# Optimization experiments

Hardware: AMD Instinct MI355X
Metric: run time of the kernel (lower is better)

Reference implementation:

```python
import jax, jax.numpy as jnp
import numpy as np

DEPTH = 3
UNITS = 512
INNER = 32          # inner_dim == F-1
F = INNER + 1
B, N = 128, 100


def setup_inputs() -> dict:
    key = jax.random.key(0)
    k1, k2, k3, k4, k5 = jax.random.split(key, 5)
    x = jax.random.normal(k1, (B, N, N, F), dtype=jnp.float32)
    # W_inner: identity tiled + small uniform noise (init_inner='identity')
    W_inner = (jnp.tile(jnp.eye(INNER, dtype=jnp.float32)[None], (DEPTH + 1, 1, 1))
               + jax.random.uniform(k2, (DEPTH + 1, INNER, INNER), minval=-0.05, maxval=0.05))
    b_inner = jax.random.uniform(k3, (DEPTH + 1, 1, INNER), minval=-0.05, maxval=0.05)
    # W_output: uniform with scale_output=0.01, tiled across depths; b_output zeros
    W_out_single = jax.random.uniform(k4, (INNER, UNITS), minval=-0.01, maxval=0.01)
    W_output = jnp.tile(W_out_single[None], (DEPTH + 1, 1, 1))
    b_output = jnp.zeros((DEPTH + 1, 1, UNITS), dtype=jnp.float32)
    return {"x": x, "W_inner": W_inner, "b_inner": b_inner,
            "W_output": W_output, "b_output": b_output}


def _fp_contribution(attr, W_output, b_output, d):
    # softmax over the units axis, per atom; attr[:, :-1] is [N, INNER]
    return jax.nn.softmax(attr[:, :-1] @ W_output[d] + b_output[d, 0], axis=-1)


def _single(graph0, W_inner, b_inner, W_output, b_output):
    # graph0: [N, N, F]
    attr = jnp.diagonal(graph0, axis1=0, axis2=1).T            # [N, F]
    fp = _fp_contribution(attr, W_output, b_output, 0).sum(axis=0)
    bonds = graph0[:, :, -1]                                    # [N, N]
    boa_T = (bonds + jnp.eye(bonds.shape[0], dtype=graph0.dtype)).T  # bonds_or_atoms transposed: [i,j]=boa[j,i]
    graph = graph0
    for d in range(1, DEPTH + 1):
        pre = graph.sum(axis=1)                                 # [N, F] row-sums of each feature slice
        core = pre[:, :-1] @ W_inner[d] + b_inner[d, 0]         # linear inner activation
        new_attr = jnp.concatenate([core, attr[:, -1:]], axis=1)  # keep bond channel
        # graph[i,j,f] += boa[j,i] * (new_attr - attr)[i,f]  (rank-1 per atom)
        graph = graph + boa_T[:, :, None] * (new_attr - attr)[:, None, :]
        attr = new_attr
        fp = fp + _fp_contribution(attr, W_output, b_output, d).sum(axis=0)
    return fp


def reference(x, W_inner, b_inner, W_output, b_output):
    return jax.vmap(lambda g: _single(g, W_inner, b_inner, W_output, b_output))(x)  # [B, UNITS]
```

## Files before the change

kernel.cpp:

```cpp
#include <hip/hip_runtime.h>

typedef __attribute__((ext_vector_type(4))) float f32x4;
typedef __attribute__((ext_vector_type(8))) short s16x8;

#define NB 128
#define NA 100
#define KF 32
#define NF 33
#define NU 512
#define ND 3

#define SZ_S0    (NB * NA * KF)
#define SZ_BONDS (NB * NA * NA)

__device__ __forceinline__ unsigned short f2bf(float f) {
    unsigned int u = __float_as_uint(f);
    u = (u + 0x7fffu + ((u >> 16) & 1u)) >> 16;
    return (unsigned short)u;
}
__device__ __forceinline__ float bf2f(unsigned short h) {
    return __uint_as_float(((unsigned int)h) << 16);
}

__global__ __launch_bounds__(256) void p1_reduce(const float* __restrict__ x,
    float* __restrict__ S0, float* __restrict__ attrAll, float* __restrict__ bonds)
{
    const int blk = blockIdx.x;
    const int b   = blk / NA;
    const int i   = blk % NA;
    const int t   = threadIdx.x;

    __shared__ float lds[NA * NF];
    __shared__ float red[8][KF];

    const float4* row4 = (const float4*)(x + (size_t)blk * (NA * NF));
    float4* lds4 = (float4*)lds;
    for (int idx = t; idx < (NA * NF) / 4; idx += 256) lds4[idx] = row4[idx];
    __syncthreads();

    const int g = t >> 5;
    const int f = t & 31;
    float p0 = 0.f, p1 = 0.f;
    for (int j = g; j + 8 < NA; j += 16) {
        p0 += lds[j * NF + f];
        p1 += lds[(j + 8) * NF + f];
    }
    if (g < 4) p0 += lds[(96 + g) * NF + f];
    red[g][f] = p0 + p1;
    __syncthreads();

    if (t < KF) {
        float s = 0.f;
#pragma unroll
        for (int gg = 0; gg < 8; ++gg) s += red[gg][t];
        S0[(size_t)blk * KF + t] = s;
    } else if (t >= 64 && t < 64 + KF) {
        attrAll[(size_t)b * (ND + 1) * NA * KF + (size_t)i * KF + (t - 64)] = lds[i * NF + (t - 64)];
    } else if (t >= 128 && t < 128 + NA) {
        const int j = t - 128;
        bonds[(size_t)blk * NA + j] = lds[j * NF + KF];
    }
}

#define NAH 50
#define ELH (NAH * KF)
__global__ __launch_bounds__(256) void p2a_recur(
    const float* __restrict__ S0, const float* __restrict__ bonds,
    const float* __restrict__ W_inner, const float* __restrict__ b_inner,
    float* __restrict__ attrAll)
{
    __shared__ float S[ELH];
    __shared__ float attr[ELH];
    __shared__ float rs[NAH];

    const int blk  = blockIdx.x;
    const int half = blk & 1;
    const int b    = blk >> 1;
    const int t    = threadIdx.x;
    const int f    = t & 31;

    const float4* s4 = (const float4*)(S0 + (size_t)b * NA * KF + half * ELH);
    const float4* a4 = (const float4*)(attrAll + (size_t)b * (ND + 1) * NA * KF + half * ELH);
    for (int idx = t; idx < ELH / 4; idx += 256) {
        ((float4*)S)[idx]    = s4[idx];
        ((float4*)attr)[idx] = a4[idx];
    }
    if (t < NAH) {
        const int i = half * NAH + t;
        const float* bb = bonds + (size_t)b * NA * NA + i;
        float c0=0.f,c1=0.f,c2=0.f,c3=0.f,c4=0.f,c5=0.f,c6=0.f,c7=0.f;
        int j = 0;
        for (; j + 8 <= NA; j += 8) {
            c0 += bb[(j+0)*NA]; c1 += bb[(j+1)*NA];
            c2 += bb[(j+2)*NA]; c3 += bb[(j+3)*NA];
            c4 += bb[(j+4)*NA]; c5 += bb[(j+5)*NA];
            c6 += bb[(j+6)*NA]; c7 += bb[(j+7)*NA];
        }
        for (; j < NA; ++j) c0 += bb[j*NA];
        rs[t] = 1.f + (((c0+c1)+(c2+c3))+((c4+c5)+(c6+c7)));
    }
    __syncthreads();

    float* attrDst = attrAll + (size_t)b * (ND + 1) * NA * KF + half * ELH;

    for (int d = 1; d <= ND; ++d) {
        float Wc[KF];
        const float* Wd = W_inner + d * KF * KF + f;
#pragma unroll
        for (int k = 0; k < KF; ++k) Wc[k] = Wd[k * KF];
        const float bi = b_inner[d * KF + f];

        float core[7];
#pragma unroll
        for (int it = 0; it < 7; ++it) {
            const int idx = t + it * 256;
            if (idx < ELH) {
                const int row = idx >> 5;
                const float4* Sr4 = (const float4*)(S + row * KF);
                float acc = bi;
#pragma unroll
                for (int q = 0; q < 8; ++q) {
                    const float4 sv = Sr4[q];
                    acc += sv.x * Wc[4*q] + sv.y * Wc[4*q+1]
                         + sv.z * Wc[4*q+2] + sv.w * Wc[4*q+3];
                }
                core[it] = acc;
            }
        }
        __syncthreads();
#pragma unroll
        for (int it = 0; it < 7; ++it) {
            const int idx = t + it * 256;
            if (idx < ELH) {
                const int row = idx >> 5;
                const float cc  = core[it];
                const float old = attr[idx];
                attr[idx] = cc;
                S[idx] += rs[row] * (cc - old);
                attrDst[(size_t)d * NA * KF + idx] = cc;
            }
        }
        __syncthreads();
    }
}

__global__ __launch_bounds__(256) void pW_prep(const float* __restrict__ W_output,
    unsigned short* __restrict__ WBh, unsigned short* __restrict__ WBl)
{
    const int i = blockIdx.x * 256 + threadIdx.x;
    const int d = i >> 14, rem = i & 16383, k = rem >> 9, col = rem & 511;
    const float v = W_output[(size_t)d * (KF * NU) + (size_t)k * NU + col];
    const unsigned short hi = f2bf(v);
    const unsigned short lo = f2bf(v - bf2f(hi));
    const int dst = d * 16384 + (col >> 4) * 512 + (k >> 3) * 128 + (col & 15) * 8 + (k & 7);
    WBh[dst] = hi;
    WBl[dst] = lo;
}

__global__ __launch_bounds__(448) void p2b_mfma(
    const float* __restrict__ attrAll,
    const unsigned short* __restrict__ WBh_g, const unsigned short* __restrict__ WBl_g,
    const float* __restrict__ b_output, float* __restrict__ fpPart)
{
    extern __shared__ unsigned char smraw[];
    unsigned short* WBh  = (unsigned short*)smraw;
    unsigned short* WBl  = WBh + 16384;
    unsigned short* aAh  = WBl + 16384;
    unsigned short* aAl  = aAh + 3584;
    float*          biasL= (float*)(aAl + 3584);
    float*          fpw  = (float*)aAh;

    const int blk = blockIdx.x;
    const int b   = blk & (NB - 1);
    const int d   = blk >> 7;
    const int t   = threadIdx.x;
    const int l   = t & 63;
    const int w   = t >> 6;

    for (int i = t; i < 2048; i += 448) ((float4*)WBh)[i] = ((const float4*)WBh_g)[d * 2048 + i];
    for (int i = t; i < 2048; i += 448) ((float4*)WBl)[i] = ((const float4*)WBl_g)[d * 2048 + i];
    for (int i = t; i < NU; i += 448)   biasL[i] = b_output[d * NU + i];

    const float* A = attrAll + ((size_t)b * (ND + 1) + d) * (NA * KF);
    for (int i = t; i < 3584; i += 448) {
        const int gr = i >> 5, k = i & 31;
        const float v = (gr < NA) ? A[gr * KF + k] : 0.f;
        const unsigned short hi = f2bf(v);
        const unsigned short lo = f2bf(v - bf2f(hi));
        const int dst = ((gr >> 4) * 4 + (k >> 3)) * 128 + (gr & 15) * 8 + (k & 7);
        aAh[dst] = hi;
        aAl[dst] = lo;
    }
    __syncthreads();

    const int aoff = (w * 4 + (l >> 4)) * 128 + (l & 15) * 8;
    const s16x8 ah = *(const s16x8*)&aAh[aoff];
    const s16x8 al = *(const s16x8*)&aAl[aoff];
    __syncthreads();

    const int laneoff = (l >> 4) * 128 + (l & 15) * 8;

    float m[4] = {-1e30f, -1e30f, -1e30f, -1e30f};
#pragma unroll 2
    for (int tt = 0; tt < 32; ++tt) {
        const s16x8 bh = *(const s16x8*)&WBh[tt * 512 + laneoff];
        f32x4 c = {0.f, 0.f, 0.f, 0.f};
        c = __builtin_amdgcn_mfma_f32_16x16x32_bf16(ah, bh, c, 0, 0, 0);
        const float bias = biasL[tt * 16 + (l & 15)];
#pragma unroll
        for (int r = 0; r < 4; ++r) m[r] = fmaxf(m[r], c[r] + bias);
    }
#pragma unroll
    for (int off = 1; off <= 8; off <<= 1)
#pragma unroll
        for (int r = 0; r < 4; ++r) m[r] = fmaxf(m[r], __shfl_xor(m[r], off, 64));

    float s[4] = {0.f, 0.f, 0.f, 0.f};
#pragma unroll 2
    for (int tt = 0; tt < 32; ++tt) {
        const s16x8 bh = *(const s16x8*)&WBh[tt * 512 + laneoff];
        const s16x8 bl = *(const s16x8*)&WBl[tt * 512 + laneoff];
        f32x4 c = {0.f, 0.f, 0.f, 0.f};
        c = __builtin_amdgcn_mfma_f32_16x16x32_bf16(ah, bh, c, 0, 0, 0);
        c = __builtin_amdgcn_mfma_f32_16x16x32_bf16(ah, bl, c, 0, 0, 0);
        c = __builtin_amdgcn_mfma_f32_16x16x32_bf16(al, bh, c, 0, 0, 0);
        const float bias = biasL[tt * 16 + (l & 15)];
#pragma unroll
        for (int r = 0; r < 4; ++r) s[r] += __expf(c[r] + bias - m[r]);
    }
#pragma unroll
    for (int off = 1; off <= 8; off <<= 1)
#pragma unroll
        for (int r = 0; r < 4; ++r) s[r] += __shfl_xor(s[r], off, 64);

    float K[4];
#pragma unroll
    for (int r = 0; r < 4; ++r) {
        const int grow = w * 16 + (l >> 4) * 4 + r;
        K[r] = (grow < NA) ? (m[r] + __logf(s[r])) : 1e30f;
    }

#pragma unroll 2
    for (int tt = 0; tt < 32; ++tt) {
        const s16x8 bh = *(const s16x8*)&WBh[tt * 512 + laneoff];
        const s16x8 bl = *(const s16x8*)&WBl[tt * 512 + laneoff];
        f32x4 c = {0.f, 0.f, 0.f, 0.f};
        c = __builtin_amdgcn_mfma_f32_16x16x32_bf16(ah, bh, c, 0, 0, 0);
        c = __builtin_amdgcn_mfma_f32_16x16x32_bf16(ah, bl, c, 0, 0, 0);
        c = __builtin_amdgcn_mfma_f32_16x16x32_bf16(al, bh, c, 0, 0, 0);
        const float bias = biasL[tt * 16 + (l & 15)];
        float f = 0.f;
#pragma unroll
        for (int r = 0; r < 4; ++r) f += __expf(c[r] + bias - K[r]);
        f += __shfl_xor(f, 16, 64);
        f += __shfl_xor(f, 32, 64);
        if (l < 16) fpw[w * NU + tt * 16 + l] = f;
    }
    __syncthreads();

    for (int u = t; u < NU; u += 448) {
        float sacc = 0.f;
#pragma unroll
        for (int ww = 0; ww < 7; ++ww) sacc += fpw[ww * NU + u];
        fpPart[((size_t)d * NB + b) * NU + u] = sacc;
    }
}

__global__ __launch_bounds__(512) void p2c_out(const float* __restrict__ fpPart,
                                               float* __restrict__ out)
{
    const int b = blockIdx.x, t = threadIdx.x;
    float s = 0.f;
#pragma unroll
    for (int d = 0; d <= ND; ++d) s += fpPart[((size_t)d * NB + b) * NU + t];
    out[(size_t)b * NU + t] = s;
}

extern "C" void kernel_launch(void* const* d_in, const int* in_sizes, int n_in,
                              void* d_out, int out_size, void* d_ws, size_t ws_size,
                              hipStream_t stream) {
    (void)in_sizes; (void)n_in; (void)out_size; (void)ws_size;
    const float* x        = (const float*)d_in[0];
    const float* W_inner  = (const float*)d_in[1];
    const float* b_inner  = (const float*)d_in[2];
    const float* W_output = (const float*)d_in[3];
    const float* b_output = (const float*)d_in[4];
    float* out = (float*)d_out;

    float* S0      = (float*)d_ws;
    float* bonds   = S0 + SZ_S0;
    float* attrAll = bonds + SZ_BONDS;
    float* fpPart  = bonds;
    unsigned short* WBh = (unsigned short*)S0;
    unsigned short* WBl = WBh + 65536;

    p1_reduce<<<NB * NA, 256, 0, stream>>>(x, S0, attrAll, bonds);
    p2a_recur<<<NB * 2, 256, 0, stream>>>(S0, bonds, W_inner, b_inner, attrAll);
    pW_prep<<<256, 256, 0, stream>>>(W_output, WBh, WBl);

    const size_t smemB = 81920;
    hipFuncSetAttribute(reinterpret_cast<const void*>(p2b_mfma),
                        hipFuncAttributeMaxDynamicSharedMemorySize, (int)smemB);
    p2b_mfma<<<NB * (ND + 1), 448, smemB, stream>>>(attrAll, WBh, WBl, b_output, fpPart);
    p2c_out<<<NB, 512, 0, stream>>>(fpPart, out);
}
```

Before: 73.34 us.

## Cache softmax exponentials in registers, fuse weight prep into recurrence kernel

The third MFMA pass that recomputed logits and exponentials is gone. Exponentials from the sum pass are now packed as bf16 pairs in registers and later scaled by the reciprocal row sum, which removes a full set of MFMAs and exps per tile. The W_output bf16 split conversion moves into extra blocks of the recurrence kernel, saving one launch; its buffer is relocated to avoid clobbering S0. This adds register pressure (64 packed values, launch bounds of 4 waves) and lowers the precision of the exponentials to bf16.

Result: faster. 69.94 us (-4.6%).

```diff
diff --git a/kernel.cpp b/kernel.cpp
--- a/kernel.cpp
+++ b/kernel.cpp
@@ -20,6 +20,11 @@
 }
 __device__ __forceinline__ float bf2f(unsigned short h) {
     return __uint_as_float(((unsigned int)h) << 16);
+}
+__device__ __forceinline__ unsigned int pack_bf16(float a, float b) {
+    const unsigned int ua = (__float_as_uint(a) + 0x8000u) >> 16;
+    const unsigned int ub = (__float_as_uint(b) + 0x8000u) & 0xffff0000u;
+    return ua | ub;
 }
 
 __global__ __launch_bounds__(256) void p1_reduce(const float* __restrict__ x,
@@ -67,16 +72,34 @@
 __global__ __launch_bounds__(256) void p2a_recur(
     const float* __restrict__ S0, const float* __restrict__ bonds,
     const float* __restrict__ W_inner, const float* __restrict__ b_inner,
-    float* __restrict__ attrAll)
+    float* __restrict__ attrAll,
+    const float* __restrict__ W_output,
+    unsigned short* __restrict__ WBh, unsigned short* __restrict__ WBl)
 {
+    const int blk = blockIdx.x;
+    const int t   = threadIdx.x;
+
+    if (blk >= NB * 2) {
+        const int base = (blk - NB * 2) * 4096;
+        for (int j = t; j < 4096; j += 256) {
+            const int i = base + j;
+            const int d = i >> 14, rem = i & 16383, k = rem >> 9, col = rem & 511;
+            const float v = W_output[(size_t)d * (KF * NU) + (size_t)k * NU + col];
+            const unsigned short hi = f2bf(v);
+            const unsigned short lo = f2bf(v - bf2f(hi));
+            const int dst = d * 16384 + (col >> 4) * 512 + (k >> 3) * 128 + (col & 15) * 8 + (k & 7);
+            WBh[dst] = hi;
+            WBl[dst] = lo;
+        }
+        return;
+    }
+
     __shared__ float S[ELH];
     __shared__ float attr[ELH];
     __shared__ float rs[NAH];
 
-    const int blk  = blockIdx.x;
     const int half = blk & 1;
     const int b    = blk >> 1;
-    const int t    = threadIdx.x;
     const int f    = t & 31;
 
     const float4* s4 = (const float4*)(S0 + (size_t)b * NA * KF + half * ELH);
@@ -144,20 +167,7 @@
     }
 }
 
-__global__ __launch_bounds__(256) void pW_prep(const float* __restrict__ W_output,
-    unsigned short* __restrict__ WBh, unsigned short* __restrict__ WBl)
-{
-    const int i = blockIdx.x * 256 + threadIdx.x;
-    const int d = i >> 14, rem = i & 16383, k = rem >> 9, col = rem & 511;
-    const float v = W_output[(size_t)d * (KF * NU) + (size_t)k * NU + col];
-    const unsigned short hi = f2bf(v);
-    const unsigned short lo = f2bf(v - bf2f(hi));
-    const int dst = d * 16384 + (col >> 4) * 512 + (k >> 3) * 128 + (col & 15) * 8 + (k & 7);
-    WBh[dst] = hi;
-    WBl[dst] = lo;
-}
-
-__global__ __launch_bounds__(448) void p2b_mfma(
+__global__ __launch_bounds__(448, 4) void p2b_mfma(
     const float* __restrict__ attrAll,
     const unsigned short* __restrict__ WBh_g, const unsigned short* __restrict__ WBl_g,
     const float* __restrict__ b_output, float* __restrict__ fpPart)
@@ -215,8 +225,9 @@
 #pragma unroll
         for (int r = 0; r < 4; ++r) m[r] = fmaxf(m[r], __shfl_xor(m[r], off, 64));
 
+    unsigned int eP[64];
     float s[4] = {0.f, 0.f, 0.f, 0.f};
-#pragma unroll 2
+#pragma unroll
     for (int tt = 0; tt < 32; ++tt) {
         const s16x8 bh = *(const s16x8*)&WBh[tt * 512 + laneoff];
         const s16x8 bl = *(const s16x8*)&WBl[tt * 512 + laneoff];
@@ -225,33 +236,34 @@
         c = __builtin_amdgcn_mfma_f32_16x16x32_bf16(ah, bl, c, 0, 0, 0);
         c = __builtin_amdgcn_mfma_f32_16x16x32_bf16(al, bh, c, 0, 0, 0);
         const float bias = biasL[tt * 16 + (l & 15)];
-#pragma unroll
-        for (int r = 0; r < 4; ++r) s[r] += __expf(c[r] + bias - m[r]);
+        const float e0 = __expf(c[0] + bias - m[0]);
+        const float e1 = __expf(c[1] + bias - m[1]);
+        const float e2 = __expf(c[2] + bias - m[2]);
+        const float e3 = __expf(c[3] + bias - m[3]);
+        s[0] += e0; s[1] += e1; s[2] += e2; s[3] += e3;
+        eP[tt * 2]     = pack_bf16(e0, e1);
+        eP[tt * 2 + 1] = pack_bf16(e2, e3);
     }
 #pragma unroll
     for (int off = 1; off <= 8; off <<= 1)
 #pragma unroll
         for (int r = 0; r < 4; ++r) s[r] += __shfl_xor(s[r], off, 64);
 
-    float K[4];
+    float inv[4];
 #pragma unroll
     for (int r = 0; r < 4; ++r) {
         const int grow = w * 16 + (l >> 4) * 4 + r;
-        K[r] = (grow < NA) ? (m[r] + __logf(s[r])) : 1e30f;
-    }
-
-#pragma unroll 2
+        inv[r] = (grow < NA) ? 1.f / s[r] : 0.f;
+    }
+
+#pragma unroll
     for (int tt = 0; tt < 32; ++tt) {
-        const s16x8 bh = *(const s16x8*)&WBh[tt * 512 + laneoff];
-        const s16x8 bl = *(const s16x8*)&WBl[tt * 512 + laneoff];
-        f32x4 c = {0.f, 0.f, 0.f, 0.f};
-        c = __builtin_amdgcn_mfma_f32_16x16x32_bf16(ah, bh, c, 0, 0, 0);
-        c = __builtin_amdgcn_mfma_f32_16x16x32_bf16(ah, bl, c, 0, 0, 0);
-        c = __builtin_amdgcn_mfma_f32_16x16x32_bf16(al, bh, c, 0, 0, 0);
-        const float bias = biasL[tt * 16 + (l & 15)];
-        float f = 0.f;
-#pragma unroll
-        for (int r = 0; r < 4; ++r) f += __expf(c[r] + bias - K[r]);
+        const unsigned int p01 = eP[tt * 2];
+        const unsigned int p23 = eP[tt * 2 + 1];
+        float f = __uint_as_float(p01 << 16)          * inv[0]
+                + __uint_as_float(p01 & 0xffff0000u)  * inv[1]
+                + __uint_as_float(p23 << 16)          * inv[2]
+                + __uint_as_float(p23 & 0xffff0000u)  * inv[3];
         f += __shfl_xor(f, 16, 64);
         f += __shfl_xor(f, 32, 64);
         if (l < 16) fpw[w * NU + tt * 16 + l] = f;
@@ -291,12 +303,12 @@
     float* bonds   = S0 + SZ_S0;
     float* attrAll = bonds + SZ_BONDS;
     float* fpPart  = bonds;
-    unsigned short* WBh = (unsigned short*)S0;
+    unsigned short* WBh = (unsigned short*)(attrAll + (size_t)NB * (ND + 1) * NA * KF);
     unsigned short* WBl = WBh + 65536;
 
     p1_reduce<<<NB * NA, 256, 0, stream>>>(x, S0, attrAll, bonds);
-    p2a_recur<<<NB * 2, 256, 0, stream>>>(S0, bonds, W_inner, b_inner, attrAll);
-    pW_prep<<<256, 256, 0, stream>>>(W_output, WBh, WBl);
+    p2a_recur<<<NB * 2 + 16, 256, 0, stream>>>(S0, bonds, W_inner, b_inner, attrAll,
+                                               W_output, WBh, WBl);
 
     const size_t smemB = 81920;
     hipFuncSetAttribute(reinterpret_cast<const void*>(p2b_mfma),
```
